# Kernel optimization log

Hardware: AMD Instinct MI355X
Metric: run time of the kernel (lower is better)

The kernel has to match this reference:

```python
import jax, jax.numpy as jnp
import numpy as np

MARKER = 50251
BETA_FLOOR = 0.1
LOCAL_SCALE = 0.3
EPS = 1e-6
WINDOW = 256

B, T, D, H, K, V = 4, 1024, 1024, 16, 64, 64
HD = D // H  # SWA head dim


def setup_inputs() -> dict:
    key = jax.random.key(0)
    ks = jax.random.split(key, 16)
    p = lambda i, shape: jax.random.normal(ks[i], shape, jnp.float32) * 0.02
    return dict(
        x=jax.random.normal(ks[0], (B, T, D), jnp.float32),
        initial_state=jnp.zeros((B, H, K, V), jnp.float32),
        W_k=p(1, (D, H * K)),
        W_v=p(2, (D, H * V)),
        W_gdn_o=p(3, (H * V, D)),
        W_beta=p(4, (D, H)), b_beta=jnp.full((H,), -2.0, jnp.float32),
        W_g=p(5, (D, H)), b_g=jnp.full((H,), 2.0, jnp.float32),
        W_lq=p(6, (D, D)), W_lk=p(7, (D, D)), W_lv=p(8, (D, D)),
        W_swa_o=p(9, (D, D)),
        W_ret_o=p(10, (H * V, D)),
        W_gate=p(11, (D, H)), b_gate=jnp.ones((H,), jnp.float32),
        norm_w=jnp.ones((D,), jnp.float32),
        input_ids=jax.random.randint(ks[12], (B, T), 0, 50257, jnp.int32),
    )


def _delta_scan(k, v, beta, g, S0):
    # gated delta rule:  Sd = g_t * S_{t-1};  S_t = Sd + beta_t * k_t (v_t - k_t Sd);  o_t = k_t S_t
    # k:[B,Tm,H,K]  v:[B,Tm,H,V]  beta,g:[B,Tm,H]  S0:[B,H,K,V]
    def step(S, inp):
        kt, vt, bt, gt = inp  # [B,H,K],[B,H,V],[B,H],[B,H]
        Sd = gt[..., None, None] * S
        err = vt - jnp.einsum('bhk,bhkv->bhv', kt, Sd)
        Sn = Sd + bt[..., None, None] * (kt[..., None] * err[:, :, None, :])
        ot = jnp.einsum('bhk,bhkv->bhv', kt, Sn)
        return Sn, ot
    Sf, o = jax.lax.scan(step, S0, (k.transpose(1, 0, 2, 3), v.transpose(1, 0, 2, 3),
                                    beta.transpose(1, 0, 2), g.transpose(1, 0, 2)))
    return o.transpose(1, 0, 2, 3), Sf  # [B,Tm,H,V], [B,H,K,V]


def _forward(x, initial_state, W_k, W_v, W_gdn_o, W_beta, b_beta, W_g, b_g,
             W_lq, W_lk, W_lv, W_swa_o, W_ret_o, W_gate, b_gate, norm_w, input_ids):
    # RMSNorm
    rms = jnp.sqrt(jnp.mean(x * x, axis=-1, keepdims=True) + EPS)
    xn = x / rms * norm_w

    # shared L2-normalized keys and values
    k_shared = (xn @ W_k).reshape(B, T, H, K)
    k_shared = k_shared / jnp.maximum(jnp.linalg.norm(k_shared, axis=-1, keepdims=True), 1e-12)
    v_full = (xn @ W_v).reshape(B, T, H, V)

    # shifted-value GDN inputs (predict next token's value)
    k = k_shared[:, :-1]
    v = v_full[:, 1:]
    beta = jax.nn.sigmoid(xn[:, :-1] @ W_beta + b_beta)  # [B,T-1,H]
    g = jax.nn.sigmoid(xn[:, :-1] @ W_g + b_g)
    marker = (input_ids[:, :-1] == MARKER)[..., None]
    beta = beta * (BETA_FLOOR + (1.0 - BETA_FLOOR) * marker.astype(beta.dtype))

    o, Sf = _delta_scan(k, v, beta, g, initial_state)
    gdn_out = jnp.concatenate([jnp.zeros((B, 1, H, V), o.dtype), o], axis=1)
    gdn_out = gdn_out.reshape(B, T, H * V) @ W_gdn_o  # [B,T,D]

    # sliding-window attention (fallback masked-softmax path)
    q = (xn @ W_lq).reshape(B, T, H, HD).transpose(0, 2, 1, 3)
    kl = (xn @ W_lk).reshape(B, T, H, HD).transpose(0, 2, 1, 3)
    vl = (xn @ W_lv).reshape(B, T, H, HD).transpose(0, 2, 1, 3)
    scale = K ** (-0.5)
    i = jnp.arange(T)[:, None]
    j = jnp.arange(T)[None, :]
    allowed = (j <= i) & (j >= i - WINDOW)  # causal within window
    attn = jnp.einsum('bhqd,bhkd->bhqk', q, kl) * scale
    attn = jnp.where(allowed, attn, -jnp.inf)
    probs = jax.nn.softmax(attn, axis=-1)
    local = jnp.einsum('bhqk,bhkd->bhqd', probs, vl).transpose(0, 2, 1, 3).reshape(B, T, D)
    local_out = LOCAL_SCALE * (local @ W_swa_o)  # eval mode

    # retrieval from final state with shared keys as queries
    retrieved = jnp.einsum('bhkv,bthk->bthv', Sf, k_shared).reshape(B, T, H * V)
    retrieval_out = retrieved @ W_ret_o
    gate = jax.nn.sigmoid(xn @ W_gate + b_gate)  # [B,T,H]
    retrieval_out = jnp.mean(gate, axis=-1, keepdims=True) * retrieval_out

    return x + gdn_out + local_out + retrieval_out


def reference(x, initial_state, W_k, W_v, W_gdn_o, W_beta, b_beta, W_g, b_g,
              W_lq, W_lk, W_lv, W_swa_o, W_ret_o, W_gate, b_gate, norm_w, input_ids):
    return _forward(x, initial_state, W_k, W_v, W_gdn_o, W_beta, b_beta, W_g, b_g,
                    W_lq, W_lk, W_lv, W_swa_o, W_ret_o, W_gate, b_gate, norm_w, input_ids)
```

## Files before the change

### kernel.cpp

```cpp
#include <hip/hip_runtime.h>
#include <hip/hip_bf16.h>

#define BB 4
#define TT 1024
#define DD 1024
#define HH 16
#define KK 64
#define VV 64
#define WIN 256
#define MARKER_ID 50251
#define PSA 5120
#define PSB 3072
#define NPROJ 5248

typedef short bfrag8 __attribute__((ext_vector_type(8)));
typedef float f32x4 __attribute__((ext_vector_type(4)));

static __device__ __forceinline__ unsigned short f2bf(float f) {
  __hip_bfloat16 h = __float2bfloat16(f);
  union { __hip_bfloat16 h; unsigned short u; } cv;
  cv.h = h;
  return cv.u;
}
static __device__ __forceinline__ float bf2f(unsigned short u) {
  union { unsigned int i; float f; } c;
  c.i = ((unsigned int)u) << 16;
  return c.f;
}
static __device__ __forceinline__ void gld_lds16(const unsigned short* g,
                                                 unsigned short* l) {
  __builtin_amdgcn_global_load_lds(
      (const __attribute__((address_space(1))) void*)g,
      (__attribute__((address_space(3))) void*)l, 16, 0, 0);
}

__global__ __launch_bounds__(256) void rmsnorm_kernel(
    const float* __restrict__ x, const float* __restrict__ nw,
    unsigned short* __restrict__ xnb) {
  int row = blockIdx.x;
  int tid = threadIdx.x;
  const float4* xr = (const float4*)(x + (size_t)row * DD);
  float4 v = xr[tid];
  float ss = v.x * v.x + v.y * v.y + v.z * v.z + v.w * v.w;
#pragma unroll
  for (int off = 32; off; off >>= 1) ss += __shfl_xor(ss, off);
  __shared__ float red[4];
  int wid = tid >> 6;
  if ((tid & 63) == 0) red[wid] = ss;
  __syncthreads();
  float tot = red[0] + red[1] + red[2] + red[3];
  float inv = 1.0f / sqrtf(tot * (1.0f / DD) + 1e-6f);
  const float4* wr = (const float4*)nw;
  float4 wv = wr[tid];
  ushort4 o;
  o.x = f2bf(v.x * inv * wv.x);
  o.y = f2bf(v.y * inv * wv.y);
  o.z = f2bf(v.z * inv * wv.z);
  o.w = f2bf(v.w * inv * wv.w);
  *(ushort4*)&xnb[(size_t)row * DD + tid * 4] = o;
}

__global__ __launch_bounds__(256) void convert_wt_kernel(
    const float* W0, const float* W1, const float* W2, const float* W3,
    const float* W4, const float* W5, const float* W6, const float* W7,
    const float* Wb, const float* Wg, const float* Wgt,
    unsigned short* C5, unsigned short* C3) {
  int tid = threadIdx.x;
  if (blockIdx.z == 8) {
    if (blockIdx.x != 0) return;
    int k0 = blockIdx.y * 64;
    for (int e = tid; e < 3 * 16 * 64; e += 256) {
      int w = e >> 10;
      int h = (e >> 6) & 15;
      int kk = e & 63;
      const float* Ws = (w == 0) ? Wb : (w == 1) ? Wg : Wgt;
      C5[(size_t)(5120 + w * 16 + h) * 1024 + k0 + kk] =
          f2bf(Ws[(size_t)(k0 + kk) * 16 + h]);
    }
    for (int e = tid; e < 80 * 64; e += 256) {
      int r = e >> 6, kk = e & 63;
      C5[(size_t)(5168 + r) * 1024 + k0 + kk] = 0;
    }
    return;
  }
  const float* W;
  unsigned short* T;
  int stride;
  float scale = 1.f;
  switch (blockIdx.z) {
    case 0: W = W0; T = C5 + 0 * 1024 * 1024; stride = 1024; break;
    case 1: W = W1; T = C5 + 1 * 1024 * 1024; stride = 1024; break;
    case 2: W = W2; T = C5 + 2 * 1024 * 1024; stride = 1024; break;
    case 3: W = W3; T = C5 + 3 * 1024 * 1024; stride = 1024; break;
    case 4: W = W4; T = C5 + 4 * 1024 * 1024; stride = 1024; break;
    case 5: W = W5; T = C3 + 0; stride = PSB; break;
    case 6: W = W6; T = C3 + 1024; stride = PSB; scale = 0.3f; break;
    default: W = W7; T = C3 + 2048; stride = PSB; break;
  }
  __shared__ float Ts[64][68];
  int n0 = blockIdx.x * 64, k0 = blockIdx.y * 64;
#pragma unroll
  for (int p = 0; p < 4; ++p) {
    int e = p * 256 + tid;
    int k = e >> 4, nq = e & 15;
    float4 w = *(const float4*)&W[(size_t)(k0 + k) * 1024 + n0 + nq * 4];
    Ts[nq * 4 + 0][k] = w.x;
    Ts[nq * 4 + 1][k] = w.y;
    Ts[nq * 4 + 2][k] = w.z;
    Ts[nq * 4 + 3][k] = w.w;
  }
  __syncthreads();
#pragma unroll
  for (int p = 0; p < 4; ++p) {
    int e = p * 256 + tid;
    int n = e >> 4, kq = e & 15;
    float4 v = *(const float4*)&Ts[n][kq * 4];
    ushort4 u;
    u.x = f2bf(v.x * scale);
    u.y = f2bf(v.y * scale);
    u.z = f2bf(v.z * scale);
    u.w = f2bf(v.w * scale);
    *(ushort4*)&T[(size_t)(n0 + n) * stride + k0 + kq * 4] = u;
  }
}

__global__ __launch_bounds__(256) void gemm_out_kernel(
    const unsigned short* __restrict__ A, const unsigned short* __restrict__ BT,
    float* __restrict__ C, const float* __restrict__ addp, int M, int N,
    int K) {
  __shared__ unsigned short As[2][128][32];
  __shared__ unsigned short Bs[2][64][32];
  int flat = blockIdx.y * gridDim.x + blockIdx.x;
  int xcd = flat & 7, local = flat >> 3;
  int m0 = (xcd * 4 + (local & 3)) * 128;
  int n0 = (local >> 2) * 64;
  int tid = threadIdx.x;
  int wave = tid >> 6, lane = tid & 63;
  int wm = wave * 32;
  int r16 = lane & 15, quad = lane >> 4;
  int lrow = lane >> 2, lcol = (lane & 3) * 8;

  f32x4 acc[2][4];
#pragma unroll
  for (int i = 0; i < 2; ++i)
#pragma unroll
    for (int j = 0; j < 4; ++j) acc[i][j] = {0.f, 0.f, 0.f, 0.f};

  auto STAGE = [&](int buf, int kt) {
#pragma unroll
    for (int q = 0; q < 2; ++q) {
      int rb = (wave * 2 + q) * 16;
      gld_lds16(&A[(size_t)(m0 + rb + lrow) * K + kt + lcol], &As[buf][rb][0]);
    }
    {
      int rb = wave * 16;
      gld_lds16(&BT[(size_t)(n0 + rb + lrow) * K + kt + lcol], &Bs[buf][rb][0]);
    }
  };
  auto COMPUTE = [&](int buf) {
    bfrag8 af[2], bq[4];
#pragma unroll
    for (int i = 0; i < 2; ++i)
      af[i] = *(const bfrag8*)&As[buf][wm + i * 16 + r16][quad * 8];
#pragma unroll
    for (int j = 0; j < 4; ++j)
      bq[j] = *(const bfrag8*)&Bs[buf][j * 16 + r16][quad * 8];
#pragma unroll
    for (int i = 0; i < 2; ++i)
#pragma unroll
      for (int j = 0; j < 4; ++j)
        acc[i][j] = __builtin_amdgcn_mfma_f32_16x16x32_bf16(af[i], bq[j],
                                                            acc[i][j], 0, 0, 0);
  };

  STAGE(0, 0);
  STAGE(1, 32);
  asm volatile("s_waitcnt vmcnt(3)" ::: "memory");
  __builtin_amdgcn_s_barrier();
  __builtin_amdgcn_sched_barrier(0);

  int cur = 0;
  for (int kt = 64; kt < K; kt += 32) {
    COMPUTE(cur);
    __builtin_amdgcn_s_barrier();
    STAGE(cur, kt);
    asm volatile("s_waitcnt vmcnt(3)" ::: "memory");
    __builtin_amdgcn_s_barrier();
    __builtin_amdgcn_sched_barrier(0);
    cur ^= 1;
  }
  COMPUTE(cur);
  asm volatile("s_waitcnt vmcnt(0)" ::: "memory");
  __builtin_amdgcn_s_barrier();
  __builtin_amdgcn_sched_barrier(0);
  COMPUTE(cur ^ 1);

#pragma unroll
  for (int i = 0; i < 2; ++i) {
#pragma unroll
    for (int r = 0; r < 4; ++r) {
      int row = m0 + wm + i * 16 + quad * 4 + r;
#pragma unroll
      for (int j = 0; j < 4; ++j) {
        int col = n0 + j * 16 + r16;
        size_t idx = (size_t)row * N + col;
        C[idx] = addp[idx] + acc[i][j][r];
      }
    }
  }
}

__global__ __launch_bounds__(256) void gemm_proj_kernel(
    const unsigned short* __restrict__ A, const unsigned short* __restrict__ BT,
    unsigned short* __restrict__ PALL, float* __restrict__ SPRJ) {
  const int K = 1024;
  __shared__ unsigned short As[2][128][32];
  __shared__ unsigned short Bs[2][128][32];
  int flat = blockIdx.y * gridDim.x + blockIdx.x;
  int xcd = flat & 7, local = flat >> 3;
  int mi = local & 3, ni = local >> 2;
  int m0 = (xcd * 4 + mi) * 128;
  int n0 = ni * 128;
  int tid = threadIdx.x;
  int wave = tid >> 6, lane = tid & 63;
  int wm = (wave & 1) * 64, wn = (wave >> 1) * 64;
  int r16 = lane & 15, quad = lane >> 4;
  int lrow = lane >> 2, lcol = (lane & 3) * 8;

  f32x4 acc[4][4];
#pragma unroll
  for (int i = 0; i < 4; ++i)
#pragma unroll
    for (int j = 0; j < 4; ++j) acc[i][j] = {0.f, 0.f, 0.f, 0.f};

  auto STAGE = [&](int buf, int kt) {
#pragma unroll
    for (int q = 0; q < 2; ++q) {
      int rb = (wave * 2 + q) * 16;
      gld_lds16(&A[(size_t)(m0 + rb + lrow) * K + kt + lcol], &As[buf][rb][0]);
      gld_lds16(&BT[(size_t)(n0 + rb + lrow) * K + kt + lcol], &Bs[buf][rb][0]);
    }
  };
  auto COMPUTE = [&](int buf) {
    bfrag8 af[4], bq[4];
#pragma unroll
    for (int i = 0; i < 4; ++i) {
      af[i] = *(const bfrag8*)&As[buf][wm + i * 16 + r16][quad * 8];
      bq[i] = *(const bfrag8*)&Bs[buf][wn + i * 16 + r16][quad * 8];
    }
#pragma unroll
    for (int i = 0; i < 4; ++i)
#pragma unroll
      for (int j = 0; j < 4; ++j)
        acc[i][j] = __builtin_amdgcn_mfma_f32_16x16x32_bf16(af[i], bq[j],
                                                            acc[i][j], 0, 0, 0);
  };

  STAGE(0, 0);
  STAGE(1, 32);
  asm volatile("s_waitcnt vmcnt(4)" ::: "memory");
  __builtin_amdgcn_s_barrier();
  __builtin_amdgcn_sched_barrier(0);

  int cur = 0;
  for (int kt = 64; kt < K; kt += 32) {
    COMPUTE(cur);
    __builtin_amdgcn_s_barrier();
    STAGE(cur, kt);
    asm volatile("s_waitcnt vmcnt(4)" ::: "memory");
    __builtin_amdgcn_s_barrier();
    __builtin_amdgcn_sched_barrier(0);
    cur ^= 1;
  }
  COMPUTE(cur);
  asm volatile("s_waitcnt vmcnt(0)" ::: "memory");
  __builtin_amdgcn_s_barrier();
  __builtin_amdgcn_sched_barrier(0);
  COMPUTE(cur ^ 1);

  bool gates = (n0 >= 5120);
#pragma unroll
  for (int i = 0; i < 4; ++i) {
#pragma unroll
    for (int r = 0; r < 4; ++r) {
      int row = m0 + wm + i * 16 + quad * 4 + r;
#pragma unroll
      for (int j = 0; j < 4; ++j) {
        int col = n0 + wn + j * 16 + r16;
        if (!gates)
          PALL[(size_t)row * PSA + col] = f2bf(acc[i][j][r]);
        else
          SPRJ[(size_t)row * 128 + col - 5120] = acc[i][j][r];
      }
    }
  }
}

__global__ __launch_bounds__(256) void gates_kernel(
    const float* __restrict__ SPRJ, const float* __restrict__ bb,
    const float* __restrict__ bg, const float* __restrict__ bgt,
    const int* __restrict__ ids, float* __restrict__ beta,
    float* __restrict__ g, float* __restrict__ mg) {
  int row = blockIdx.x * 4 + (threadIdx.x >> 6);
  int lane = threadIdx.x & 63;
  if (lane < 48) {
    int h = lane & 15;
    float v = SPRJ[(size_t)row * 128 + lane];
    float bias = (lane < 16) ? bb[h] : (lane < 32) ? bg[h] : bgt[h];
    float s = 1.f / (1.f + __expf(-(v + bias)));
    if (lane < 16) {
      float mk = (ids[row] == MARKER_ID) ? 1.f : 0.1f;
      beta[(size_t)row * 16 + h] = s * mk;
    } else if (lane < 32) {
      g[(size_t)row * 16 + h] = s;
    } else {
      float sum = s;
#pragma unroll
      for (int off = 1; off < 16; off <<= 1) sum += __shfl_xor(sum, off);
      if (lane == 32) mg[row] = sum * (1.f / 16.f);
    }
  }
}

__global__ __launch_bounds__(256) void knorm_kernel(
    unsigned short* __restrict__ pall) {
  int w = blockIdx.x * 4 + (threadIdx.x >> 6);
  int lane = threadIdx.x & 63;
  size_t addr = (size_t)(w >> 4) * PSA + (w & 15) * 64 + lane;
  float v = bf2f(pall[addr]);
  float ss = v * v;
#pragma unroll
  for (int off = 32; off; off >>= 1) ss += __shfl_xor(ss, off);
  float n = sqrtf(ss);
  n = fmaxf(n, 1e-12f);
  pall[addr] = f2bf(v / n);
}

__global__ __launch_bounds__(256) void attn_mfma_kernel(
    const unsigned short* __restrict__ PALL, unsigned short* __restrict__ ACAT) {
  __shared__ unsigned short Qs[64][72];
  __shared__ unsigned short Ks[64][72];
  __shared__ unsigned short Vt[64][72];
  __shared__ unsigned short Ps[64][72];
  int qb = blockIdx.x * 64;
  int bh = blockIdx.y;
  int h = bh & 15, b = bh >> 4;
  int tid = threadIdx.x, lane = tid & 63, wave = tid >> 6;
  int r16 = lane & 15, quad = lane >> 4;
  int m0w = wave * 16;
  const unsigned short* Qg = PALL + (size_t)b * TT * PSA + 2048 + h * 64;
  const unsigned short* Kg = Qg + 1024;
  const unsigned short* Vg = Qg + 2048;
  int sr = tid >> 2, sq = tid & 3;
  {
    *(uint4*)&Qs[sr][sq * 16] =
        *(const uint4*)&Qg[(size_t)(qb + sr) * PSA + sq * 16];
    *(uint4*)&Qs[sr][sq * 16 + 8] =
        *(const uint4*)&Qg[(size_t)(qb + sr) * PSA + sq * 16 + 8];
  }
  float m[4], l[4];
  f32x4 o[4];
#pragma unroll
  for (int r = 0; r < 4; ++r) {
    m[r] = -1e30f;
    l[r] = 0.f;
    o[r] = {0.f, 0.f, 0.f, 0.f};
  }
  int kt0 = qb - (int)WIN;
  if (kt0 < 0) kt0 = 0;

  for (int kt = kt0; kt <= qb; kt += 64) {
    __syncthreads();
    {
      *(uint4*)&Ks[sr][sq * 16] =
          *(const uint4*)&Kg[(size_t)(kt + sr) * PSA + sq * 16];
      *(uint4*)&Ks[sr][sq * 16 + 8] =
          *(const uint4*)&Kg[(size_t)(kt + sr) * PSA + sq * 16 + 8];
      union { uint4 u4[2]; unsigned short s[16]; } vv;
      vv.u4[0] = *(const uint4*)&Vg[(size_t)(kt + sr) * PSA + sq * 16];
      vv.u4[1] = *(const uint4*)&Vg[(size_t)(kt + sr) * PSA + sq * 16 + 8];
#pragma unroll
      for (int i = 0; i < 16; ++i) Vt[sq * 16 + i][sr] = vv.s[i];
    }
    __syncthreads();
    bfrag8 af0 = *(const bfrag8*)&Qs[m0w + r16][quad * 8];
    bfrag8 af1 = *(const bfrag8*)&Qs[m0w + r16][quad * 8 + 32];
    f32x4 s[4];
#pragma unroll
    for (int j = 0; j < 4; ++j) s[j] = {0.f, 0.f, 0.f, 0.f};
#pragma unroll
    for (int j = 0; j < 4; ++j) {
      bfrag8 b0 = *(const bfrag8*)&Ks[j * 16 + r16][quad * 8];
      bfrag8 b1 = *(const bfrag8*)&Ks[j * 16 + r16][quad * 8 + 32];
      s[j] = __builtin_amdgcn_mfma_f32_16x16x32_bf16(af0, b0, s[j], 0, 0, 0);
      s[j] = __builtin_amdgcn_mfma_f32_16x16x32_bf16(af1, b1, s[j], 0, 0, 0);
    }
    bool oldest = (kt == qb - (int)WIN);
    bool newest = (kt == qb);
#pragma unroll
    for (int r = 0; r < 4; ++r) {
      int il = m0w + quad * 4 + r;
      float sv[4];
#pragma unroll
      for (int j = 0; j < 4; ++j) {
        int jl = j * 16 + r16;
        float v = s[j][r] * 0.125f;
        if (oldest && jl < il) v = -1e30f;
        if (newest && jl > il) v = -1e30f;
        sv[j] = v;
      }
      float mx = fmaxf(fmaxf(sv[0], sv[1]), fmaxf(sv[2], sv[3]));
#pragma unroll
      for (int off = 1; off < 16; off <<= 1) mx = fmaxf(mx, __shfl_xor(mx, off));
      float mn = fmaxf(m[r], mx);
      float al = __expf(m[r] - mn);
      m[r] = mn;
      float rs = 0.f;
#pragma unroll
      for (int j = 0; j < 4; ++j) {
        float p = __expf(sv[j] - mn);
        rs += p;
        Ps[il][j * 16 + r16] = f2bf(p);
      }
#pragma unroll
      for (int off = 1; off < 16; off <<= 1) rs += __shfl_xor(rs, off);
      l[r] = l[r] * al + rs;
#pragma unroll
      for (int j = 0; j < 4; ++j) o[j][r] *= al;
    }
    bfrag8 pa0 = *(const bfrag8*)&Ps[m0w + r16][quad * 8];
    bfrag8 pa1 = *(const bfrag8*)&Ps[m0w + r16][quad * 8 + 32];
#pragma unroll
    for (int j = 0; j < 4; ++j) {
      bfrag8 v0 = *(const bfrag8*)&Vt[j * 16 + r16][quad * 8];
      bfrag8 v1 = *(const bfrag8*)&Vt[j * 16 + r16][quad * 8 + 32];
      o[j] = __builtin_amdgcn_mfma_f32_16x16x32_bf16(pa0, v0, o[j], 0, 0, 0);
      o[j] = __builtin_amdgcn_mfma_f32_16x16x32_bf16(pa1, v1, o[j], 0, 0, 0);
    }
  }
#pragma unroll
  for (int r = 0; r < 4; ++r) {
    int row = m0w + quad * 4 + r;
    float inv = 1.f / l[r];
#pragma unroll
    for (int j = 0; j < 4; ++j) {
      ACAT[((size_t)(b * TT + qb + row)) * PSB + 1024 + h * 64 + j * 16 + r16] =
          f2bf(o[j][r] * inv);
    }
  }
}

__global__ __launch_bounds__(256) void scan_phaseA(
    const unsigned short* __restrict__ PALL, const float* __restrict__ beta,
    const float* __restrict__ g, unsigned short* __restrict__ UFg,
    unsigned short* __restrict__ Zg, unsigned short* __restrict__ Pg,
    unsigned short* __restrict__ Qg, float* __restrict__ Ag) {
  __shared__ unsigned short Kc[64][72];
  __shared__ unsigned short KTb[64][72];
  __shared__ float Vc[64][68];
  __shared__ float Msv[64][68];
  __shared__ unsigned short UFT[64][72];
  __shared__ unsigned short ZTl[64][72];
  __shared__ float aArr[64], iaArr[64], bArr[64], baArr[64], sKT[64];
  __shared__ float aCs;

  int c = blockIdx.x, bh = blockIdx.y;
  int b = bh >> 4, h = bh & 15;
  int tc = c * 64;
  int tid = threadIdx.x, lane = tid & 63, wave = tid >> 6;
  int r16 = lane & 15, quad = lane >> 4;
  int m0w = wave * 16;
  size_t bhc = (size_t)bh * 16 + c;

  const unsigned short* kbase = PALL + ((size_t)b * TT) * PSA + h * 64;
  const unsigned short* vbase = kbase + 1024;
  const float* bbase = beta + ((size_t)b * TT) * HH + h;
  const float* gbase = g + ((size_t)b * TT) * HH + h;

  if (tid < 64) {
    int ts = tc + tid;
    bool pad = (ts > 1022);
    float gv = pad ? 1.f : gbase[(size_t)ts * HH];
    float bv = pad ? 0.f : bbase[(size_t)ts * HH];
    float p = gv;
#pragma unroll
    for (int o = 1; o < 64; o <<= 1) {
      float t = __shfl_up(p, o);
      if (lane >= o) p *= t;
    }
    aArr[tid] = p;
    iaArr[tid] = 1.f / p;
    bArr[tid] = bv;
    baArr[tid] = bv * p;
    float aC = __shfl(p, 63);
    sKT[tid] = aC / p;
    if (tid == 0) aCs = aC;
    Ag[bhc * 64 + tid] = p;
  }
  __syncthreads();
  {
    int r = tid >> 2, q = tid & 3;
    int ts = tc + r;
    float skt = sKT[r];
    union { uint4 u4[2]; unsigned short s[16]; } kv;
    kv.u4[0] = *(const uint4*)&kbase[(size_t)ts * PSA + q * 16];
    kv.u4[1] = *(const uint4*)&kbase[(size_t)ts * PSA + q * 16 + 8];
    *(uint4*)&Kc[r][q * 16] = kv.u4[0];
    *(uint4*)&Kc[r][q * 16 + 8] = kv.u4[1];
#pragma unroll
    for (int i = 0; i < 16; ++i)
      KTb[q * 16 + i][r] = f2bf(bf2f(kv.s[i]) * skt);
    if (ts <= 1022) {
      union { uint4 u4[2]; unsigned short s[16]; } vv;
      vv.u4[0] = *(const uint4*)&vbase[(size_t)(ts + 1) * PSA + q * 16];
      vv.u4[1] = *(const uint4*)&vbase[(size_t)(ts + 1) * PSA + q * 16 + 8];
#pragma unroll
      for (int i = 0; i < 16; ++i) Vc[r][q * 16 + i] = bf2f(vv.s[i]);
    } else {
#pragma unroll
      for (int i = 0; i < 16; ++i) Vc[r][q * 16 + i] = 0.f;
    }
  }
  __syncthreads();
  {
    bfrag8 af0 = *(const bfrag8*)&Kc[m0w + r16][quad * 8];
    bfrag8 af1 = *(const bfrag8*)&Kc[m0w + r16][quad * 8 + 32];
    f32x4 acc1[4];
#pragma unroll
    for (int j = 0; j < 4; ++j) acc1[j] = {0.f, 0.f, 0.f, 0.f};
#pragma unroll
    for (int j = 0; j < 4; ++j) {
      bfrag8 k0 = *(const bfrag8*)&Kc[j * 16 + r16][quad * 8];
      bfrag8 k1 = *(const bfrag8*)&Kc[j * 16 + r16][quad * 8 + 32];
      acc1[j] = __builtin_amdgcn_mfma_f32_16x16x32_bf16(af0, k0, acc1[j], 0, 0, 0);
      acc1[j] = __builtin_amdgcn_mfma_f32_16x16x32_bf16(af1, k1, acc1[j], 0, 0, 0);
    }
#pragma unroll
    for (int j = 0; j < 4; ++j) {
#pragma unroll
      for (int r = 0; r < 4; ++r) {
        int row = m0w + quad * 4 + r;
        int col = j * 16 + r16;
        Msv[row][col] =
            (col < row) ? bArr[row] * aArr[row] * iaArr[col] * acc1[j][r] : 0.f;
      }
    }
  }
  __syncthreads();
  if (wave < 2) {
    float u[64];
    if (wave == 0) {
#pragma unroll
      for (int t = 0; t < 64; ++t) u[t] = bArr[t] * Vc[t][lane];
    } else {
#pragma unroll
      for (int t = 0; t < 64; ++t) u[t] = baArr[t] * bf2f(Kc[t][lane]);
    }
#pragma unroll
    for (int t = 1; t < 64; ++t) {
      float a0 = 0.f, a1 = 0.f, a2 = 0.f, a3 = 0.f;
#pragma unroll
      for (int s4 = 0; s4 * 4 < t; ++s4) {
        float4 mr = *(const float4*)&Msv[t][s4 * 4];
        a0 = fmaf(mr.x, u[s4 * 4 + 0], a0);
        a1 = fmaf(mr.y, u[s4 * 4 + 1], a1);
        a2 = fmaf(mr.z, u[s4 * 4 + 2], a2);
        a3 = fmaf(mr.w, u[s4 * 4 + 3], a3);
      }
      u[t] -= (a0 + a1) + (a2 + a3);
    }
    unsigned short* Tls = (wave == 0) ? &UFT[lane][0] : &ZTl[lane][0];
#pragma unroll
    for (int t2 = 0; t2 < 32; ++t2) {
      unsigned int pk = (unsigned int)f2bf(u[2 * t2]) |
                        ((unsigned int)f2bf(u[2 * t2 + 1]) << 16);
      *(unsigned int*)&Tls[2 * t2] = pk;
    }
    unsigned short* Gn = (wave == 0) ? UFg : Zg;
#pragma unroll
    for (int t = 0; t < 64; ++t) {
      Gn[(bhc * 64 + t) * 64 + lane] = f2bf(u[t]);
    }
  }
  __syncthreads();
  {
    bfrag8 af0 = *(const bfrag8*)&KTb[m0w + r16][quad * 8];
    bfrag8 af1 = *(const bfrag8*)&KTb[m0w + r16][quad * 8 + 32];
    f32x4 accp[4], accq[4];
#pragma unroll
    for (int j = 0; j < 4; ++j) {
      accp[j] = {0.f, 0.f, 0.f, 0.f};
      accq[j] = {0.f, 0.f, 0.f, 0.f};
    }
#pragma unroll
    for (int j = 0; j < 4; ++j) {
      bfrag8 z0 = *(const bfrag8*)&ZTl[j * 16 + r16][quad * 8];
      bfrag8 z1 = *(const bfrag8*)&ZTl[j * 16 + r16][quad * 8 + 32];
      accp[j] = __builtin_amdgcn_mfma_f32_16x16x32_bf16(af0, z0, accp[j], 0, 0, 0);
      accp[j] = __builtin_amdgcn_mfma_f32_16x16x32_bf16(af1, z1, accp[j], 0, 0, 0);
      bfrag8 u0 = *(const bfrag8*)&UFT[j * 16 + r16][quad * 8];
      bfrag8 u1 = *(const bfrag8*)&UFT[j * 16 + r16][quad * 8 + 32];
      accq[j] = __builtin_amdgcn_mfma_f32_16x16x32_bf16(af0, u0, accq[j], 0, 0, 0);
      accq[j] = __builtin_amdgcn_mfma_f32_16x16x32_bf16(af1, u1, accq[j], 0, 0, 0);
    }
    float aC = aCs;
#pragma unroll
    for (int j = 0; j < 4; ++j) {
#pragma unroll
      for (int r = 0; r < 4; ++r) {
        int row = m0w + quad * 4 + r;
        int col = j * 16 + r16;
        float pv = ((row == col) ? aC : 0.f) - accp[j][r];
        Pg[bhc * 4096 + (size_t)row * 64 + col] = f2bf(pv);
        Qg[bhc * 4096 + (size_t)row * 64 + col] = f2bf(accq[j][r]);
      }
    }
  }
}

__global__ __launch_bounds__(256) void scan_phaseB(
    const float* __restrict__ S0, const unsigned short* __restrict__ Pg,
    const unsigned short* __restrict__ Qg, unsigned short* __restrict__ SinTg,
    float* __restrict__ Sf, unsigned short* __restrict__ ACAT) {
  __shared__ unsigned short STb[64][72];
  __shared__ unsigned short Pl[64][72];
  int bh = blockIdx.x;
  int b = bh >> 4, h = bh & 15;
  int tid = threadIdx.x, lane = tid & 63, wave = tid >> 6;
  int r16 = lane & 15, quad = lane >> 4;
  int m0w = wave * 16;
  int rr = tid >> 2, qq = tid & 3;
  {
    const float* s0p = S0 + (size_t)bh * 4096;
#pragma unroll
    for (int i = 0; i < 4; ++i) {
      float4 sv = *(const float4*)&s0p[rr * 64 + qq * 16 + i * 4];
      STb[qq * 16 + i * 4 + 0][rr] = f2bf(sv.x);
      STb[qq * 16 + i * 4 + 1][rr] = f2bf(sv.y);
      STb[qq * 16 + i * 4 + 2][rr] = f2bf(sv.z);
      STb[qq * 16 + i * 4 + 3][rr] = f2bf(sv.w);
    }
    if (tid < 64) ACAT[((size_t)b * TT) * PSB + h * 64 + tid] = 0;
  }
  for (int c = 0; c < 16; ++c) {
    size_t bhc = (size_t)bh * 16 + c;
    __syncthreads();
    {
      uint4 s0v = *(const uint4*)&STb[rr][qq * 16];
      uint4 s1v = *(const uint4*)&STb[rr][qq * 16 + 8];
      *(uint4*)&SinTg[bhc * 4096 + (size_t)rr * 64 + qq * 16] = s0v;
      *(uint4*)&SinTg[bhc * 4096 + (size_t)rr * 64 + qq * 16 + 8] = s1v;
      uint4 p0 = *(const uint4*)&Pg[bhc * 4096 + (size_t)rr * 64 + qq * 16];
      uint4 p1 = *(const uint4*)&Pg[bhc * 4096 + (size_t)rr * 64 + qq * 16 + 8];
      *(uint4*)&Pl[rr][qq * 16] = p0;
      *(uint4*)&Pl[rr][qq * 16 + 8] = p1;
    }
    __syncthreads();
    f32x4 acc[4];
#pragma unroll
    for (int j = 0; j < 4; ++j) acc[j] = {0.f, 0.f, 0.f, 0.f};
    {
      bfrag8 af0 = *(const bfrag8*)&Pl[m0w + r16][quad * 8];
      bfrag8 af1 = *(const bfrag8*)&Pl[m0w + r16][quad * 8 + 32];
#pragma unroll
      for (int j = 0; j < 4; ++j) {
        bfrag8 s0v = *(const bfrag8*)&STb[j * 16 + r16][quad * 8];
        bfrag8 s1v = *(const bfrag8*)&STb[j * 16 + r16][quad * 8 + 32];
        acc[j] = __builtin_amdgcn_mfma_f32_16x16x32_bf16(af0, s0v, acc[j], 0, 0, 0);
        acc[j] = __builtin_amdgcn_mfma_f32_16x16x32_bf16(af1, s1v, acc[j], 0, 0, 0);
      }
    }
    float snew[4][4];
#pragma unroll
    for (int j = 0; j < 4; ++j) {
#pragma unroll
      for (int r = 0; r < 4; ++r) {
        int row = m0w + quad * 4 + r;
        int col = j * 16 + r16;
        snew[j][r] = acc[j][r] + bf2f(Qg[bhc * 4096 + (size_t)row * 64 + col]);
      }
    }
    __syncthreads();
#pragma unroll
    for (int j = 0; j < 4; ++j) {
#pragma unroll
      for (int r = 0; r < 4; ++r) {
        int row = m0w + quad * 4 + r;
        int col = j * 16 + r16;
        STb[col][row] = f2bf(snew[j][r]);
        if (c == 15) Sf[(size_t)bh * 4096 + (size_t)row * 64 + col] = snew[j][r];
      }
    }
  }
}

__global__ __launch_bounds__(256) void scan_phaseC(
    const unsigned short* __restrict__ PALL,
    const unsigned short* __restrict__ UFg,
    const unsigned short* __restrict__ Zg,
    const unsigned short* __restrict__ SinTg, const float* __restrict__ Ag,
    unsigned short* __restrict__ ACAT) {
  __shared__ unsigned short Kc[64][72];
  __shared__ unsigned short SvT[64][72];
  __shared__ unsigned short Zl[64][72];
  __shared__ unsigned short Ufl[64][72];
  __shared__ unsigned short Wl[64][72];
  __shared__ unsigned short UTl[64][72];
  __shared__ float aA[64], iaA[64];

  int c = blockIdx.x, bh = blockIdx.y;
  int b = bh >> 4, h = bh & 15;
  int tc = c * 64;
  int tid = threadIdx.x, lane = tid & 63, wave = tid >> 6;
  int r16 = lane & 15, quad = lane >> 4;
  int m0w = wave * 16;
  size_t bhc = (size_t)bh * 16 + c;
  const unsigned short* kbase = PALL + ((size_t)b * TT) * PSA + h * 64;

  if (tid < 64) {
    float av = Ag[bhc * 64 + tid];
    aA[tid] = av;
    iaA[tid] = 1.f / av;
  }
  {
    int r = tid >> 2, q = tid & 3;
    int ts = tc + r;
    *(uint4*)&Kc[r][q * 16] = *(const uint4*)&kbase[(size_t)ts * PSA + q * 16];
    *(uint4*)&Kc[r][q * 16 + 8] =
        *(const uint4*)&kbase[(size_t)ts * PSA + q * 16 + 8];
    uint4 sv0 = *(const uint4*)&SinTg[bhc * 4096 + (size_t)r * 64 + q * 16];
    uint4 sv1 = *(const uint4*)&SinTg[bhc * 4096 + (size_t)r * 64 + q * 16 + 8];
    *(uint4*)&SvT[r][q * 16] = sv0;
    *(uint4*)&SvT[r][q * 16 + 8] = sv1;
    uint4 zv0 = *(const uint4*)&Zg[(bhc * 64 + r) * 64 + q * 16];
    uint4 zv1 = *(const uint4*)&Zg[(bhc * 64 + r) * 64 + q * 16 + 8];
    *(uint4*)&Zl[r][q * 16] = zv0;
    *(uint4*)&Zl[r][q * 16 + 8] = zv1;
    uint4 uv0 = *(const uint4*)&UFg[(bhc * 64 + r) * 64 + q * 16];
    uint4 uv1 = *(const uint4*)&UFg[(bhc * 64 + r) * 64 + q * 16 + 8];
    *(uint4*)&Ufl[r][q * 16] = uv0;
    *(uint4*)&Ufl[r][q * 16 + 8] = uv1;
  }
  __syncthreads();
  float op[4][4];
  {
    bfrag8 af0 = *(const bfrag8*)&Kc[m0w + r16][quad * 8];
    bfrag8 af1 = *(const bfrag8*)&Kc[m0w + r16][quad * 8 + 32];
    bfrag8 zf0 = *(const bfrag8*)&Zl[m0w + r16][quad * 8];
    bfrag8 zf1 = *(const bfrag8*)&Zl[m0w + r16][quad * 8 + 32];
    f32x4 acc1[4], acc2[4], acc3[4];
#pragma unroll
    for (int j = 0; j < 4; ++j) {
      acc1[j] = {0.f, 0.f, 0.f, 0.f};
      acc2[j] = {0.f, 0.f, 0.f, 0.f};
      acc3[j] = {0.f, 0.f, 0.f, 0.f};
    }
#pragma unroll
    for (int j = 0; j < 4; ++j) {
      bfrag8 k0 = *(const bfrag8*)&Kc[j * 16 + r16][quad * 8];
      bfrag8 k1 = *(const bfrag8*)&Kc[j * 16 + r16][quad * 8 + 32];
      acc1[j] = __builtin_amdgcn_mfma_f32_16x16x32_bf16(af0, k0, acc1[j], 0, 0, 0);
      acc1[j] = __builtin_amdgcn_mfma_f32_16x16x32_bf16(af1, k1, acc1[j], 0, 0, 0);
      bfrag8 s0 = *(const bfrag8*)&SvT[j * 16 + r16][quad * 8];
      bfrag8 s1 = *(const bfrag8*)&SvT[j * 16 + r16][quad * 8 + 32];
      acc3[j] = __builtin_amdgcn_mfma_f32_16x16x32_bf16(af0, s0, acc3[j], 0, 0, 0);
      acc3[j] = __builtin_amdgcn_mfma_f32_16x16x32_bf16(af1, s1, acc3[j], 0, 0, 0);
      acc2[j] = __builtin_amdgcn_mfma_f32_16x16x32_bf16(zf0, s0, acc2[j], 0, 0, 0);
      acc2[j] = __builtin_amdgcn_mfma_f32_16x16x32_bf16(zf1, s1, acc2[j], 0, 0, 0);
    }
#pragma unroll
    for (int j = 0; j < 4; ++j) {
#pragma unroll
      for (int r = 0; r < 4; ++r) {
        int row = m0w + quad * 4 + r;
        int col = j * 16 + r16;
        Wl[row][col] = (col <= row) ? f2bf(aA[row] * iaA[col] * acc1[j][r])
                                    : (unsigned short)0;
        float uval = bf2f(Ufl[row][col]) - acc2[j][r];
        UTl[col][row] = f2bf(uval);
        op[j][r] = aA[row] * acc3[j][r];
      }
    }
  }
  __syncthreads();
  {
    bfrag8 wf0 = *(const bfrag8*)&Wl[m0w + r16][quad * 8];
    bfrag8 wf1 = *(const bfrag8*)&Wl[m0w + r16][quad * 8 + 32];
    f32x4 acc4[4];
#pragma unroll
    for (int j = 0; j < 4; ++j) acc4[j] = {0.f, 0.f, 0.f, 0.f};
#pragma unroll
    for (int j = 0; j < 4; ++j) {
      bfrag8 u0 = *(const bfrag8*)&UTl[j * 16 + r16][quad * 8];
      bfrag8 u1 = *(const bfrag8*)&UTl[j * 16 + r16][quad * 8 + 32];
      acc4[j] = __builtin_amdgcn_mfma_f32_16x16x32_bf16(wf0, u0, acc4[j], 0, 0, 0);
      acc4[j] = __builtin_amdgcn_mfma_f32_16x16x32_bf16(wf1, u1, acc4[j], 0, 0, 0);
    }
#pragma unroll
    for (int j = 0; j < 4; ++j) {
#pragma unroll
      for (int r = 0; r < 4; ++r) {
        int row = m0w + quad * 4 + r;
        int col = j * 16 + r16;
        int ts = tc + row;
        if (ts < 1023) {
          ACAT[((size_t)b * TT + ts + 1) * PSB + h * 64 + col] =
              f2bf(op[j][r] + acc4[j][r]);
        }
      }
    }
  }
}

__global__ __launch_bounds__(256) void retrieve_kernel(
    const unsigned short* __restrict__ PALL, const float* __restrict__ Sf,
    const float* __restrict__ mg, unsigned short* __restrict__ ACAT) {
  int w = blockIdx.x * 4 + (threadIdx.x >> 6);
  int lane = threadIdx.x & 63;
  int bt = w >> 4;
  float kl = bf2f(PALL[(size_t)bt * PSA + (w & 15) * 64 + lane]);
  int b = bt >> 10;
  int bh = b * 16 + (w & 15);
  const float* sfp = Sf + (size_t)bh * 4096;
  float acc = 0.f;
#pragma unroll
  for (int k = 0; k < 64; ++k) {
    float kk = __shfl(kl, k);
    acc = fmaf(kk, sfp[k * 64 + lane], acc);
  }
  ACAT[(size_t)bt * PSB + 2048 + (w & 15) * 64 + lane] = f2bf(acc * mg[bt]);
}

extern "C" void kernel_launch(void* const* d_in, const int* in_sizes, int n_in,
                              void* d_out, int out_size, void* d_ws,
                              size_t ws_size, hipStream_t stream) {
  (void)in_sizes; (void)n_in; (void)out_size; (void)ws_size;
  const float* x       = (const float*)d_in[0];
  const float* S0      = (const float*)d_in[1];
  const float* W_k     = (const float*)d_in[2];
  const float* W_v     = (const float*)d_in[3];
  const float* W_gdn_o = (const float*)d_in[4];
  const float* W_beta  = (const float*)d_in[5];
  const float* b_beta  = (const float*)d_in[6];
  const float* W_g     = (const float*)d_in[7];
  const float* b_g     = (const float*)d_in[8];
  const float* W_lq    = (const float*)d_in[9];
  const float* W_lk    = (const float*)d_in[10];
  const float* W_lv    = (const float*)d_in[11];
  const float* W_swa_o = (const float*)d_in[12];
  const float* W_ret_o = (const float*)d_in[13];
  const float* W_gate  = (const float*)d_in[14];
  const float* b_gate  = (const float*)d_in[15];
  const float* norm_w  = (const float*)d_in[16];
  const int*   ids     = (const int*)d_in[17];
  float* out = (float*)d_out;

  char* ws = (char*)d_ws;
  size_t off = 0;
  auto allocf = [&](size_t n) {
    float* p = (float*)(ws + off);
    off += n * sizeof(float);
    return p;
  };
  auto allocu = [&](size_t n) {
    unsigned short* p = (unsigned short*)(ws + off);
    off += n * sizeof(unsigned short);
    return p;
  };
  const int M = BB * TT;
  unsigned short* XNb    = allocu((size_t)M * DD);
  unsigned short* PALL   = allocu((size_t)M * PSA);
  unsigned short* ACAT   = allocu((size_t)M * PSB);
  float*          SPRJ   = allocf((size_t)M * 128);
  unsigned short* WTcat5 = allocu((size_t)NPROJ * 1024);
  unsigned short* WTcat3 = allocu((size_t)1024 * PSB);
  float* BETA = allocf((size_t)M * HH);
  float* Gg   = allocf((size_t)M * HH);
  float* MG   = allocf((size_t)M);
  float* SF   = allocf((size_t)BB * HH * KK * VV);
  const size_t CH = (size_t)BB * HH * 16 * 64 * 64;
  unsigned short* UFg   = allocu(CH);
  unsigned short* Zg    = allocu(CH);
  unsigned short* Pg    = allocu(CH);
  unsigned short* Qg    = allocu(CH);
  unsigned short* SinTg = allocu(CH);
  float* Ag = allocf((size_t)BB * HH * 16 * 64);

  rmsnorm_kernel<<<M, 256, 0, stream>>>(x, norm_w, XNb);

  convert_wt_kernel<<<dim3(16, 16, 9), 256, 0, stream>>>(
      W_k, W_v, W_lq, W_lk, W_lv, W_gdn_o, W_swa_o, W_ret_o, W_beta, W_g,
      W_gate, WTcat5, WTcat3);

  gemm_proj_kernel<<<dim3(41, 32), 256, 0, stream>>>(XNb, WTcat5, PALL, SPRJ);

  knorm_kernel<<<(M * HH) / 4, 256, 0, stream>>>(PALL);
  gates_kernel<<<M / 4, 256, 0, stream>>>(SPRJ, b_beta, b_g, b_gate, ids, BETA,
                                          Gg, MG);

  scan_phaseA<<<dim3(16, BB * HH), 256, 0, stream>>>(PALL, BETA, Gg, UFg, Zg,
                                                     Pg, Qg, Ag);
  scan_phaseB<<<BB * HH, 256, 0, stream>>>(S0, Pg, Qg, SinTg, SF, ACAT);
  scan_phaseC<<<dim3(16, BB * HH), 256, 0, stream>>>(PALL, UFg, Zg, SinTg, Ag,
                                                     ACAT);

  attn_mfma_kernel<<<dim3(TT / 64, BB * HH), 256, 0, stream>>>(PALL, ACAT);

  retrieve_kernel<<<(M * HH) / 4, 256, 0, stream>>>(PALL, SF, MG, ACAT);

  gemm_out_kernel<<<dim3(16, 32), 256, 0, stream>>>(ACAT, WTcat3, out, x, M, DD,
                                                    3072);
}
```

Measured before the change: 386.8 us.

## Restructure projection GEMM pipeline to single-barrier prefetch and raise occupancy bound

```diff
diff --git a/kernel.cpp b/kernel.cpp
--- a/kernel.cpp
+++ b/kernel.cpp
@@ -210,7 +210,7 @@
   }
 }
 
-__global__ __launch_bounds__(256) void gemm_proj_kernel(
+__global__ __launch_bounds__(256, 4) void gemm_proj_kernel(
     const unsigned short* __restrict__ A, const unsigned short* __restrict__ BT,
     unsigned short* __restrict__ PALL, float* __restrict__ SPRJ) {
   const int K = 1024;
@@ -233,20 +233,29 @@
 #pragma unroll
     for (int j = 0; j < 4; ++j) acc[i][j] = {0.f, 0.f, 0.f, 0.f};
 
-  auto STAGE = [&](int buf, int kt) {
+#pragma unroll
+  for (int q = 0; q < 2; ++q) {
+    int rb = (wave * 2 + q) * 16;
+    gld_lds16(&A[(size_t)(m0 + rb + lrow) * K + lcol], &As[0][rb][0]);
+    gld_lds16(&BT[(size_t)(n0 + rb + lrow) * K + lcol], &Bs[0][rb][0]);
+  }
+  __syncthreads();
+
+  int cur = 0;
+  for (int kt = 32; kt < K; kt += 32) {
 #pragma unroll
     for (int q = 0; q < 2; ++q) {
       int rb = (wave * 2 + q) * 16;
-      gld_lds16(&A[(size_t)(m0 + rb + lrow) * K + kt + lcol], &As[buf][rb][0]);
-      gld_lds16(&BT[(size_t)(n0 + rb + lrow) * K + kt + lcol], &Bs[buf][rb][0]);
-    }
-  };
-  auto COMPUTE = [&](int buf) {
+      gld_lds16(&A[(size_t)(m0 + rb + lrow) * K + kt + lcol],
+                &As[cur ^ 1][rb][0]);
+      gld_lds16(&BT[(size_t)(n0 + rb + lrow) * K + kt + lcol],
+                &Bs[cur ^ 1][rb][0]);
+    }
     bfrag8 af[4], bq[4];
 #pragma unroll
     for (int i = 0; i < 4; ++i) {
-      af[i] = *(const bfrag8*)&As[buf][wm + i * 16 + r16][quad * 8];
-      bq[i] = *(const bfrag8*)&Bs[buf][wn + i * 16 + r16][quad * 8];
+      af[i] = *(const bfrag8*)&As[cur][wm + i * 16 + r16][quad * 8];
+      bq[i] = *(const bfrag8*)&Bs[cur][wn + i * 16 + r16][quad * 8];
     }
 #pragma unroll
     for (int i = 0; i < 4; ++i)
@@ -254,30 +263,23 @@
       for (int j = 0; j < 4; ++j)
         acc[i][j] = __builtin_amdgcn_mfma_f32_16x16x32_bf16(af[i], bq[j],
                                                             acc[i][j], 0, 0, 0);
-  };
-
-  STAGE(0, 0);
-  STAGE(1, 32);
-  asm volatile("s_waitcnt vmcnt(4)" ::: "memory");
-  __builtin_amdgcn_s_barrier();
-  __builtin_amdgcn_sched_barrier(0);
-
-  int cur = 0;
-  for (int kt = 64; kt < K; kt += 32) {
-    COMPUTE(cur);
-    __builtin_amdgcn_s_barrier();
-    STAGE(cur, kt);
-    asm volatile("s_waitcnt vmcnt(4)" ::: "memory");
-    __builtin_amdgcn_s_barrier();
-    __builtin_amdgcn_sched_barrier(0);
+    __syncthreads();
     cur ^= 1;
   }
-  COMPUTE(cur);
-  asm volatile("s_waitcnt vmcnt(0)" ::: "memory");
-  __builtin_amdgcn_s_barrier();
-  __builtin_amdgcn_sched_barrier(0);
-  COMPUTE(cur ^ 1);
-
+  {
+    bfrag8 af[4], bq[4];
+#pragma unroll
+    for (int i = 0; i < 4; ++i) {
+      af[i] = *(const bfrag8*)&As[cur][wm + i * 16 + r16][quad * 8];
+      bq[i] = *(const bfrag8*)&Bs[cur][wn + i * 16 + r16][quad * 8];
+    }
+#pragma unroll
+    for (int i = 0; i < 4; ++i)
+#pragma unroll
+      for (int j = 0; j < 4; ++j)
+        acc[i][j] = __builtin_amdgcn_mfma_f32_16x16x32_bf16(af[i], bq[j],
+                                                            acc[i][j], 0, 0, 0);
+  }
   bool gates = (n0 >= 5120);
 #pragma unroll
   for (int i = 0; i < 4; ++i) {
```

Result: no change. 385.0 us (-0.4%).
